# Kernel optimization log

Hardware: AMD Instinct MI355X
Metric: run time of the kernel (lower is better)

## Reference

```python
import jax, jax.numpy as jnp
import numpy as np

N_NODES = 20000
NUM_STEPS = 6
SIGNS = (1.0, -1.0, 1.0, -1.0, 1.0, -1.0)  # TF_POS, TF_NEG, PPI_POS, PPI_NEG, UNDIR, MIRNA_NEG


def setup_inputs() -> dict:
    key = jax.random.key(0)
    ks = jax.random.split(key, 12)
    B, N, E, H, C = 64, N_NODES, 400000, 64, 32
    return {
        "ctl_base": jax.random.normal(ks[0], (B, N), jnp.float32),
        "u_raw": jax.random.normal(ks[1], (B, N), jnp.float32),
        "cell_idx": jax.random.randint(ks[2], (B,), 0, C, jnp.int32),
        "edge_src": jax.random.randint(ks[3], (6, E), 0, N, jnp.int32),
        "edge_dst": jax.random.randint(ks[4], (6, E), 0, N, jnp.int32),
        "edge_val": jax.random.uniform(ks[5], (6, E), jnp.float32),
        "g_logits": jnp.zeros((6,), jnp.float32),
        "alpha_logits": jnp.zeros((NUM_STEPS,), jnp.float32),
        "cell_emb": jax.random.normal(ks[6], (C, H), jnp.float32),
        "W1": jax.random.normal(ks[7], (3, H), jnp.float32) * 0.1,
        "b1": jnp.zeros((H,), jnp.float32),
        "W2": jax.random.normal(ks[8], (H, 1), jnp.float32) * 0.1,
        "b2": jnp.zeros((1,), jnp.float32),
    }


def _spmm_right(h, src, dst, val):
    # out[b, j] = sum_{e: dst[e]==j} h[b, src[e]] * val[e]   (== h @ A)
    gathered = h.T[src] * val[:, None]  # [E, B]
    return jax.ops.segment_sum(gathered, dst, num_segments=N_NODES).T  # [B, N]


def reference(ctl_base, u_raw, g_logits, alpha_logits, cell_emb,
              W1, b1, W2, b2, edge_val, edge_src, edge_dst, cell_idx):
    g = jax.nn.softplus(g_logits)          # [6] relation gates
    alphas = jax.nn.sigmoid(alpha_logits)  # [num_steps]
    h0 = u_raw
    h = u_raw
    for k in range(NUM_STEPS):
        msg = jnp.zeros_like(h)
        for r in range(6):
            msg = msg + SIGNS[r] * g[r] * _spmm_right(h, edge_src[r], edge_dst[r], edge_val[r])
        a = alphas[k]
        h = a * h0 + (1.0 - a) * msg
    # decode: stack [ctl, u_raw, hK] -> [B, N, 3]
    x = jnp.stack([ctl_base, u_raw, h], axis=-1)
    hd = jax.nn.relu(jnp.einsum('bnf,fh->bnh', x, W1) + b1)  # [B, N, H]
    hd = hd + cell_emb[cell_idx][:, None, :]
    y = (jnp.einsum('bnh,ho->bno', hd, W2) + b2)[..., 0]  # [B, N]
    return y
```

## Files before the change

kernel.cpp:

```cpp
#include <hip/hip_runtime.h>

#define N_NODES 20000
#define HID 64
#define NSTEPS 6
#define NSLICE 8
#define SLICE_SZ (N_NODES / NSLICE)
#define SUBB 64
#define NBLK (NSLICE * SUBB)
#define TBLK ((N_NODES + 63) / 64)
#define NB1 512
#define CBLK ((N_NODES + 255) / 256)
#define MAGIC 13422

typedef _Float16 h8_t __attribute__((ext_vector_type(8)));
typedef unsigned u4_t __attribute__((ext_vector_type(4)));

union U16H { unsigned short u; _Float16 h; };
union U4H8 { uint4 u; _Float16 h[8]; };

__device__ __forceinline__ _Float16 us_as_h(unsigned short s) { U16H u; u.u = s; return u.h; }
__device__ __forceinline__ unsigned short h_as_us(_Float16 h) { U16H u; u.h = h; return u.u; }

__device__ __forceinline__ int slice_of(int d) {
    return (int)(((unsigned)d * (unsigned)MAGIC) >> 25);
}
__device__ __forceinline__ float softplusf_(float x) {
    return (x > 0.f) ? (x + log1pf(expf(-x))) : log1pf(expf(x));
}
__device__ __forceinline__ float sigmoidf_(float x) {
    return 1.f / (1.f + expf(-x));
}

__global__ __launch_bounds__(256) void count8_kernel(const int* __restrict__ edst,
                                                     int* __restrict__ gcnt, int TE,
                                                     u4_t* __restrict__ egq, long long egq_n) {
    u4_t z = {0u, 0u, 0u, 0u};
    for (long long i = (long long)blockIdx.x * 256 + threadIdx.x; i < egq_n;
         i += (long long)NB1 * 256)
        __builtin_nontemporal_store(z, egq + i);

    __shared__ int lh[8];
    int bk = blockIdx.x;
    int lane = threadIdx.x & 63;
    if (threadIdx.x < 8) lh[threadIdx.x] = 0;
    __syncthreads();
    int chunk = ((TE + NB1 - 1) / NB1 + 255) & ~255;
    int lo = bk * chunk;
    int hi = min(lo + chunk, TE);
    int my = 0;
    for (int ii = 0; ii < chunk; ii += 256) {
        int i = lo + ii + (int)threadIdx.x;
        bool act = i < hi;
        int s = -1;
        if (act) s = slice_of(__builtin_nontemporal_load(edst + i));
#pragma unroll
        for (int q = 0; q < 8; ++q) {
            unsigned long long b = __ballot(s == q);
            if (lane == q) my += (int)__popcll(b);
        }
    }
    if (lane < 8) atomicAdd(&lh[lane], my);
    __syncthreads();
    if (threadIdx.x < 8) gcnt[bk * 8 + threadIdx.x] = lh[threadIdx.x];
}

__global__ __launch_bounds__(256) void scan8_kernel(const int* __restrict__ gcnt,
                                                    int* __restrict__ blkoff,
                                                    int* __restrict__ bbase,
                                                    const float* __restrict__ g_logits,
                                                    const float* __restrict__ alpha_logits,
                                                    const int* __restrict__ cell_idx,
                                                    const float* __restrict__ cell_emb,
                                                    const float* __restrict__ W2,
                                                    const float* __restrict__ b2,
                                                    float* __restrict__ gsign,
                                                    float* __restrict__ alph,
                                                    float* __restrict__ cell_dot) {
    __shared__ int psum[8][33];
    int tid = threadIdx.x;
    int s = tid >> 5, g = tid & 31;
    const int per = NB1 / 32;
    int sum = 0;
    for (int b = g * per; b < (g + 1) * per; ++b) sum += gcnt[b * 8 + s];
    psum[s][g] = sum;
    __syncthreads();
    if (tid < 8) {
        int run = 0;
        for (int i = 0; i < 32; ++i) { int v = psum[tid][i]; psum[tid][i] = run; run += v; }
        psum[tid][32] = run;
    }
    __syncthreads();
    int run = psum[s][g];
    for (int b = g * per; b < (g + 1) * per; ++b) {
        blkoff[b * 8 + s] = run;
        run += gcnt[b * 8 + s];
    }
    if (tid == 0) {
        int acc = 0;
        bbase[0] = 0;
        for (int q = 0; q < 8; ++q) { acc += psum[q][32]; bbase[q + 1] = acc; }
    }
    if (tid < 64) {
        if (tid < 6) gsign[tid] = ((tid & 1) ? -1.f : 1.f) * softplusf_(g_logits[tid]);
        if (tid < NSTEPS) alph[tid] = sigmoidf_(alpha_logits[tid]);
        int ci = cell_idx[tid];
        float acc = b2[0];
        for (int hh = 0; hh < HID; ++hh) acc = fmaf(cell_emb[ci * HID + hh], W2[hh], acc);
        cell_dot[tid] = acc;
    }
}

__global__ __launch_bounds__(256) void bucket_kernel(const int* __restrict__ esrc,
                                                     const int* __restrict__ edst,
                                                     const float* __restrict__ eval,
                                                     const float* __restrict__ gsign,
                                                     const int* __restrict__ blkoff,
                                                     const int* __restrict__ bbase,
                                                     int2* __restrict__ bucket,
                                                     int E, int TE) {
    __shared__ int lcur[8];
    int bk = blockIdx.x;
    int lane = threadIdx.x & 63;
    if (threadIdx.x < 8) lcur[threadIdx.x] = bbase[threadIdx.x] + blkoff[bk * 8 + threadIdx.x];
    __syncthreads();
    int chunk = ((TE + NB1 - 1) / NB1 + 255) & ~255;
    int lo = bk * chunk;
    int hi = min(lo + chunk, TE);
    for (int ii = 0; ii < chunk; ii += 256) {
        int i = lo + ii + (int)threadIdx.x;
        bool act = i < hi;
        int s = -1, meta = 0, cb = 0;
        if (act) {
            int d  = __builtin_nontemporal_load(edst + i);
            int sv = __builtin_nontemporal_load(esrc + i);
            float ev = __builtin_nontemporal_load(eval + i);
            s = slice_of(d);
            int dl = d - s * SLICE_SZ;
            meta = sv | (dl << 16);
            int r = (i >= E) + (i >= 2 * E) + (i >= 3 * E) + (i >= 4 * E) + (i >= 5 * E);
            cb = __float_as_int(gsign[r] * ev);
        }
        int pos = 0;
#pragma unroll
        for (int q = 0; q < 8; ++q) {
            unsigned long long b = __ballot(s == q);
            if (b) {
                int leader = (int)__ffsll(b) - 1;
                int base = 0;
                if (lane == leader) base = atomicAdd(&lcur[q], (int)__popcll(b));
                base = __shfl(base, leader);
                if (s == q) pos = base + (int)__popcll(b & ((1ull << lane) - 1ull));
            }
        }
        if (act) bucket[pos] = make_int2(meta, cb);
    }
}

__global__ __launch_bounds__(256) void hist2db_kernel(const int2* __restrict__ bucket,
                                                      const int* __restrict__ bbase,
                                                      int* __restrict__ blkcnt) {
    __shared__ int lh[SLICE_SZ];
    int bk = blockIdx.x;
    int slice = bk & (NSLICE - 1);
    int sub = bk >> 3;
    for (int b = threadIdx.x; b < SLICE_SZ; b += 256) lh[b] = 0;
    __syncthreads();
    int lo = bbase[slice];
    int total = bbase[slice + 1] - lo;
    int chunk = ((total + SUBB - 1) / SUBB + 255) & ~255;
    int beg = lo + sub * chunk;
    int end = min(beg + chunk, lo + total);
    const int* mp = (const int*)bucket;
    for (int i = beg + (int)threadIdx.x; i < end; i += 256) {
        int meta = __builtin_nontemporal_load(mp + 2 * (size_t)i);
        atomicAdd(&lh[((unsigned)meta) >> 16], 1);
    }
    __syncthreads();
    int* out = blkcnt + (size_t)(slice * SUBB + sub) * SLICE_SZ;
    for (int b = threadIdx.x; b < SLICE_SZ; b += 256) out[b] = lh[b];
}

__global__ __launch_bounds__(256) void colscan_kernel(int* __restrict__ blkcnt,
                                                      int* __restrict__ counts,
                                                      int* __restrict__ blksum) {
    int n = blockIdx.x * 256 + threadIdx.x;
    int run = 0;
    if (n < N_NODES) {
        int slice = n / SLICE_SZ, bin = n % SLICE_SZ;
        size_t base = (size_t)slice * SUBB * SLICE_SZ + bin;
#pragma unroll 8
        for (int s = 0; s < SUBB; ++s) {
            size_t idx = base + (size_t)s * SLICE_SZ;
            int t = blkcnt[idx];
            blkcnt[idx] = run;
            run += t;
        }
        counts[n] = run;
    }
    int g = (n < N_NODES) ? ((run + 7) >> 3) : 0;
#pragma unroll
    for (int st = 1; st < 64; st <<= 1) g += __shfl_xor(g, st, 64);
    __shared__ int wsum[4];
    if ((threadIdx.x & 63) == 0) wsum[threadIdx.x >> 6] = g;
    __syncthreads();
    if (threadIdx.x == 0) blksum[blockIdx.x] = wsum[0] + wsum[1] + wsum[2] + wsum[3];
}

__global__ __launch_bounds__(256) void scan2_kernel(const int* __restrict__ counts,
                                                    const int* __restrict__ blksum,
                                                    int* __restrict__ grp_ptr, int n) {
    int b = blockIdx.x;
    int tid = threadIdx.x, lane = tid & 63, wid = tid >> 6;
    int i = b * 256 + tid;
    int v = (i < n) ? ((counts[i] + 7) >> 3) : 0;
    int x = v;
#pragma unroll
    for (int st = 1; st < 64; st <<= 1) {
        int t = __shfl_up(x, st, 64);
        if (lane >= st) x += t;
    }
    __shared__ int wsum[4];
    if (lane == 63) wsum[wid] = x;
    int s = ((lane < b) ? blksum[lane] : 0) +
            ((lane + 64 < b) ? blksum[lane + 64] : 0);
#pragma unroll
    for (int st = 1; st < 64; st <<= 1) s += __shfl_xor(s, st, 64);
    __syncthreads();
    int woff = s;
    if (wid > 0) woff += wsum[0];
    if (wid > 1) woff += wsum[1];
    if (wid > 2) woff += wsum[2];
    int off = woff + x - v;
    if (i < n) grp_ptr[i] = off;
    if (i == n - 1) grp_ptr[n] = off + v;
}

__global__ __launch_bounds__(256) void scatter2b_kernel(const int2* __restrict__ bucket,
                                                        const int* __restrict__ bbase,
                                                        const int* __restrict__ grp_ptr,
                                                        const int* __restrict__ blkcnt,
                                                        unsigned* __restrict__ eg,
                                                        const float* __restrict__ u_raw,
                                                        float* __restrict__ u_t,
                                                        _Float16* __restrict__ uh) {
    __shared__ float smem[64 * 65];
    int bk = blockIdx.x;
    if (bk >= NBLK) {
        float(*tile)[65] = (float(*)[65])smem;
        int c0 = (bk - NBLK) * 64;
        int tx = threadIdx.x & 63, ty = threadIdx.x >> 6;
#pragma unroll
        for (int i = 0; i < 16; ++i) {
            int c = c0 + tx;
            tile[ty + i * 4][tx] = (c < N_NODES) ? u_raw[(size_t)(ty + i * 4) * N_NODES + c] : 0.f;
        }
        __syncthreads();
#pragma unroll
        for (int i = 0; i < 16; ++i) {
            int c = c0 + ty + i * 4;
            if (c < N_NODES) {
                float v = tile[tx][ty + i * 4];
                u_t[(size_t)c * 64 + tx] = v;
                uh[(size_t)c * 64 + tx] = (_Float16)v;
            }
        }
        return;
    }
    int* lbase = (int*)smem;
    int slice = bk & (NSLICE - 1);
    int sub = bk >> 3;
    int lo_n = slice * SLICE_SZ;
    const int* boff = blkcnt + (size_t)(slice * SUBB + sub) * SLICE_SZ;
    for (int b = threadIdx.x; b < SLICE_SZ; b += 256)
        lbase[b] = grp_ptr[lo_n + b] * 8 + boff[b];
    __syncthreads();
    int lo = bbase[slice];
    int total = bbase[slice + 1] - lo;
    int chunk = ((total + SUBB - 1) / SUBB + 255) & ~255;
    int beg = lo + sub * chunk;
    int end = min(beg + chunk, lo + total);
    for (int i = beg + (int)threadIdx.x; i < end; i += 256) {
        long long rec = __builtin_nontemporal_load((const long long*)bucket + i);
        int meta = (int)rec;
        float cf = __int_as_float((int)(rec >> 32));
        int pos = atomicAdd(&lbase[((unsigned)meta) >> 16], 1);
        eg[pos] = (unsigned)(meta & 0xFFFF) | ((unsigned)h_as_us((_Float16)cf) << 16);
    }
}

__global__ __launch_bounds__(256) void step_kernel(const _Float16* __restrict__ h_in,
                                                   const float* __restrict__ h0,
                                                   _Float16* __restrict__ h_out,
                                                   float* __restrict__ hF,
                                                   const int* __restrict__ grp_ptr,
                                                   const unsigned* __restrict__ eg,
                                                   const float* __restrict__ alph,
                                                   int k, int last) {
    int lane = threadIdx.x & 63;
    int node = blockIdx.x * 4 + (threadIdx.x >> 6);
    if (node >= N_NODES) return;
    int gb = __builtin_amdgcn_readfirstlane(grp_ptr[node]);
    int ge = __builtin_amdgcn_readfirstlane(grp_ptr[node + 1]);
    int sub8 = lane >> 3;
    const _Float16* hbase = h_in + (lane & 7) * 8;
    const unsigned* ep = eg + sub8;
    float acc[8] = {0.f, 0.f, 0.f, 0.f, 0.f, 0.f, 0.f, 0.f};
    int g = gb;
    unsigned e0, e1, e2, e3;
    if (g + 4 <= ge) {
        e0 = ep[(size_t)g * 8];
        e1 = ep[(size_t)g * 8 + 8];
        e2 = ep[(size_t)g * 8 + 16];
        e3 = ep[(size_t)g * 8 + 24];
    }
    for (; g + 8 <= ge; g += 4) {
        h8_t v0 = *(const h8_t*)(hbase + (e0 & 0xFFFFu) * 64);
        h8_t v1 = *(const h8_t*)(hbase + (e1 & 0xFFFFu) * 64);
        h8_t v2 = *(const h8_t*)(hbase + (e2 & 0xFFFFu) * 64);
        h8_t v3 = *(const h8_t*)(hbase + (e3 & 0xFFFFu) * 64);
        unsigned f0 = ep[(size_t)(g + 4) * 8];
        unsigned f1 = ep[(size_t)(g + 4) * 8 + 8];
        unsigned f2 = ep[(size_t)(g + 4) * 8 + 16];
        unsigned f3 = ep[(size_t)(g + 4) * 8 + 24];
        float c0 = (float)us_as_h((unsigned short)(e0 >> 16));
        float c1 = (float)us_as_h((unsigned short)(e1 >> 16));
        float c2 = (float)us_as_h((unsigned short)(e2 >> 16));
        float c3 = (float)us_as_h((unsigned short)(e3 >> 16));
#pragma unroll
        for (int j = 0; j < 8; ++j) acc[j] = fmaf((float)v0[j], c0, acc[j]);
#pragma unroll
        for (int j = 0; j < 8; ++j) acc[j] = fmaf((float)v1[j], c1, acc[j]);
#pragma unroll
        for (int j = 0; j < 8; ++j) acc[j] = fmaf((float)v2[j], c2, acc[j]);
#pragma unroll
        for (int j = 0; j < 8; ++j) acc[j] = fmaf((float)v3[j], c3, acc[j]);
        e0 = f0; e1 = f1; e2 = f2; e3 = f3;
    }
    if (g + 4 <= ge) {
        h8_t v0 = *(const h8_t*)(hbase + (e0 & 0xFFFFu) * 64);
        h8_t v1 = *(const h8_t*)(hbase + (e1 & 0xFFFFu) * 64);
        h8_t v2 = *(const h8_t*)(hbase + (e2 & 0xFFFFu) * 64);
        h8_t v3 = *(const h8_t*)(hbase + (e3 & 0xFFFFu) * 64);
        float c0 = (float)us_as_h((unsigned short)(e0 >> 16));
        float c1 = (float)us_as_h((unsigned short)(e1 >> 16));
        float c2 = (float)us_as_h((unsigned short)(e2 >> 16));
        float c3 = (float)us_as_h((unsigned short)(e3 >> 16));
#pragma unroll
        for (int j = 0; j < 8; ++j) acc[j] = fmaf((float)v0[j], c0, acc[j]);
#pragma unroll
        for (int j = 0; j < 8; ++j) acc[j] = fmaf((float)v1[j], c1, acc[j]);
#pragma unroll
        for (int j = 0; j < 8; ++j) acc[j] = fmaf((float)v2[j], c2, acc[j]);
#pragma unroll
        for (int j = 0; j < 8; ++j) acc[j] = fmaf((float)v3[j], c3, acc[j]);
        g += 4;
    }
    for (; g < ge; ++g) {
        unsigned e = ep[(size_t)g * 8];
        h8_t v = *(const h8_t*)(hbase + (e & 0xFFFFu) * 64);
        float c = (float)us_as_h((unsigned short)(e >> 16));
#pragma unroll
        for (int j = 0; j < 8; ++j) acc[j] = fmaf((float)v[j], c, acc[j]);
    }
#pragma unroll
    for (int st = 8; st < 64; st <<= 1) {
#pragma unroll
        for (int j = 0; j < 8; ++j) acc[j] += __shfl_xor(acc[j], st, 64);
    }
    if (lane < 8) {
        float a = alph[k];
        int base = node * 64 + lane * 8;
        float4 h0a = *(const float4*)(h0 + base);
        float4 h0b = *(const float4*)(h0 + base + 4);
        float om = 1.f - a;
        float r0 = fmaf(a, h0a.x, om * acc[0]);
        float r1 = fmaf(a, h0a.y, om * acc[1]);
        float r2 = fmaf(a, h0a.z, om * acc[2]);
        float r3 = fmaf(a, h0a.w, om * acc[3]);
        float r4 = fmaf(a, h0b.x, om * acc[4]);
        float r5 = fmaf(a, h0b.y, om * acc[5]);
        float r6 = fmaf(a, h0b.z, om * acc[6]);
        float r7 = fmaf(a, h0b.w, om * acc[7]);
        if (last) {
            *(float4*)(hF + base)     = make_float4(r0, r1, r2, r3);
            *(float4*)(hF + base + 4) = make_float4(r4, r5, r6, r7);
        } else {
            U4H8 o;
            o.h[0] = (_Float16)r0; o.h[1] = (_Float16)r1;
            o.h[2] = (_Float16)r2; o.h[3] = (_Float16)r3;
            o.h[4] = (_Float16)r4; o.h[5] = (_Float16)r5;
            o.h[6] = (_Float16)r6; o.h[7] = (_Float16)r7;
            *(uint4*)(h_out + base) = o.u;
        }
    }
}

__global__ __launch_bounds__(256) void decode_kernel(float* __restrict__ y,
                                                     const float* __restrict__ ctl,
                                                     const float* __restrict__ u,
                                                     const float* __restrict__ hF,
                                                     const float* __restrict__ W1,
                                                     const float* __restrict__ b1,
                                                     const float* __restrict__ W2,
                                                     const float* __restrict__ cell_dot) {
    __shared__ float tile[64][65];
    __shared__ float4 pack[HID];
    __shared__ float w2s[HID];
    __shared__ float cds[64];
    if (threadIdx.x < HID) {
        int hh = threadIdx.x;
        pack[hh] = make_float4(W1[0 * HID + hh], W1[1 * HID + hh], W1[2 * HID + hh], b1[hh]);
        w2s[hh] = W2[hh];
        cds[hh] = cell_dot[hh];
    }
    int n0 = blockIdx.x * 64;
    int tx = threadIdx.x & 63, ty = threadIdx.x >> 6;
#pragma unroll
    for (int i = 0; i < 16; ++i) {
        int n = n0 + ty + i * 4;
        tile[ty + i * 4][tx] = (n < N_NODES) ? hF[(size_t)n * 64 + tx] : 0.f;
    }
    __syncthreads();
#pragma unroll
    for (int i = 0; i < 16; ++i) {
        int b = ty + i * 4;
        int n = n0 + tx;
        if (n < N_NODES) {
            size_t idx = (size_t)b * N_NODES + n;
            float xc = ctl[idx], xu = u[idx], xh = tile[tx][b];
            float acc = 0.f;
#pragma unroll 8
            for (int hh = 0; hh < HID; ++hh) {
                float4 p = pack[hh];
                float t = fmaf(xc, p.x, fmaf(xu, p.y, fmaf(xh, p.z, p.w)));
                t = fmaxf(t, 0.f);
                acc = fmaf(t, w2s[hh], acc);
            }
            y[idx] = acc + cds[b];
        }
    }
}

extern "C" void kernel_launch(void* const* d_in, const int* in_sizes, int n_in,
                              void* d_out, int out_size, void* d_ws, size_t ws_size,
                              hipStream_t stream) {
    const float* ctl          = (const float*)d_in[0];
    const float* u_raw        = (const float*)d_in[1];
    const int*   cell_idx     = (const int*)d_in[2];
    const int*   edge_src     = (const int*)d_in[3];
    const int*   edge_dst     = (const int*)d_in[4];
    const float* edge_val     = (const float*)d_in[5];
    const float* g_logits     = (const float*)d_in[6];
    const float* alpha_logits = (const float*)d_in[7];
    const float* cell_emb     = (const float*)d_in[8];
    const float* W1           = (const float*)d_in[9];
    const float* b1           = (const float*)d_in[10];
    const float* W2           = (const float*)d_in[11];
    const float* b2           = (const float*)d_in[12];
    float* y = (float*)d_out;

    const int TE = in_sizes[3];
    const int E  = TE / 6;
    const int NB = N_NODES * 64;

    char* ws = (char*)d_ws;
    size_t off = 0;
    auto alloc = [&](size_t bytes) -> char* {
        char* p = ws + off;
        off += (bytes + 255) & ~(size_t)255;
        return p;
    };
    int* grp_ptr = (int*)alloc((N_NODES + 1) * sizeof(int));
    int* counts  = (int*)alloc(N_NODES * sizeof(int));
    int* blksum  = (int*)alloc(CBLK * sizeof(int));
    int* blkcnt  = (int*)alloc((size_t)NSLICE * SUBB * SLICE_SZ * sizeof(int));
    int* gcnt    = (int*)alloc((size_t)NB1 * 8 * sizeof(int));
    int* blkoff  = (int*)alloc((size_t)NB1 * 8 * sizeof(int));
    int* bbase   = (int*)alloc(16 * sizeof(int));
    const size_t MAXG = (size_t)TE / 8 + N_NODES + 8;
    unsigned* eg = (unsigned*)alloc(MAXG * 8 * sizeof(unsigned));
    int2* bucket    = (int2*)alloc((size_t)TE * sizeof(int2));
    _Float16* uh    = (_Float16*)alloc((size_t)NB * 2);
    _Float16* hA    = (_Float16*)alloc((size_t)NB * 2);
    _Float16* hB    = (_Float16*)alloc((size_t)NB * 2);
    float* hF       = (float*)alloc((size_t)NB * 4);
    float* u_t      = (float*)alloc((size_t)NB * sizeof(float));
    float* gsign    = (float*)alloc(8 * sizeof(float));
    float* alph     = (float*)alloc(8 * sizeof(float));
    float* cell_dot = (float*)alloc(64 * sizeof(float));

    count8_kernel<<<NB1, 256, 0, stream>>>(edge_dst, gcnt, TE,
                                           (u4_t*)eg, (long long)(MAXG * 2));
    scan8_kernel<<<1, 256, 0, stream>>>(gcnt, blkoff, bbase, g_logits, alpha_logits,
                                        cell_idx, cell_emb, W2, b2,
                                        gsign, alph, cell_dot);
    bucket_kernel<<<NB1, 256, 0, stream>>>(edge_src, edge_dst, edge_val, gsign,
                                           blkoff, bbase, bucket, E, TE);
    hist2db_kernel<<<NBLK, 256, 0, stream>>>(bucket, bbase, blkcnt);
    colscan_kernel<<<CBLK, 256, 0, stream>>>(blkcnt, counts, blksum);
    scan2_kernel<<<CBLK, 256, 0, stream>>>(counts, blksum, grp_ptr, N_NODES);
    scatter2b_kernel<<<NBLK + TBLK, 256, 0, stream>>>(bucket, bbase, grp_ptr, blkcnt,
                                                      eg, u_raw, u_t, uh);

    const _Float16* hin = uh;
    for (int k = 0; k < NSTEPS; ++k) {
        _Float16* hout = (k & 1) ? hB : hA;
        step_kernel<<<(N_NODES + 3) / 4, 256, 0, stream>>>(hin, u_t, hout, hF, grp_ptr,
                                                           eg, alph, k, k == NSTEPS - 1);
        hin = hout;
    }

    decode_kernel<<<TBLK, 256, 0, stream>>>(y, ctl, u_raw, hF, W1, b1, W2, cell_dot);
}
```

Before: 341.3 us.

## Interleave edge groups into 32-edge quads for uint4 edge loads and deeper gather pipelining

Edge lists per node are padded to multiples of 32 and written in an interleaved order so each 8-lane subgroup can fetch four consecutive edges with one 128-bit load. The step kernel is rewritten into a two-stage software pipeline that keeps two sets of four gathered h rows in flight while the edge loads for the next stages are prefetched. This aims to cut the number of edge-load instructions and hide gather latency. The cost is more padding (up to 31 extra zero edges per node), which adds wasted gathers, a larger edge buffer, and higher register use.

Measured after the change: 352.7 us. 1.03x slower.

```diff
diff --git a/kernel.cpp b/kernel.cpp
--- a/kernel.cpp
+++ b/kernel.cpp
@@ -197,7 +197,7 @@
         }
         counts[n] = run;
     }
-    int g = (n < N_NODES) ? ((run + 7) >> 3) : 0;
+    int g = (n < N_NODES) ? (((run + 31) >> 5) << 2) : 0;
 #pragma unroll
     for (int st = 1; st < 64; st <<= 1) g += __shfl_xor(g, st, 64);
     __shared__ int wsum[4];
@@ -212,7 +212,7 @@
     int b = blockIdx.x;
     int tid = threadIdx.x, lane = tid & 63, wid = tid >> 6;
     int i = b * 256 + tid;
-    int v = (i < n) ? ((counts[i] + 7) >> 3) : 0;
+    int v = (i < n) ? (((counts[i] + 31) >> 5) << 2) : 0;
     int x = v;
 #pragma unroll
     for (int st = 1; st < 64; st <<= 1) {
@@ -267,12 +267,16 @@
         return;
     }
     int* lbase = (int*)smem;
+    int* sbase = (int*)smem + SLICE_SZ;
     int slice = bk & (NSLICE - 1);
     int sub = bk >> 3;
     int lo_n = slice * SLICE_SZ;
     const int* boff = blkcnt + (size_t)(slice * SUBB + sub) * SLICE_SZ;
-    for (int b = threadIdx.x; b < SLICE_SZ; b += 256)
-        lbase[b] = grp_ptr[lo_n + b] * 8 + boff[b];
+    for (int b = threadIdx.x; b < SLICE_SZ; b += 256) {
+        int gp = grp_ptr[lo_n + b] * 8;
+        sbase[b] = gp;
+        lbase[b] = gp + boff[b];
+    }
     __syncthreads();
     int lo = bbase[slice];
     int total = bbase[slice + 1] - lo;
@@ -283,8 +287,12 @@
         long long rec = __builtin_nontemporal_load((const long long*)bucket + i);
         int meta = (int)rec;
         float cf = __int_as_float((int)(rec >> 32));
-        int pos = atomicAdd(&lbase[((unsigned)meta) >> 16], 1);
-        eg[pos] = (unsigned)(meta & 0xFFFF) | ((unsigned)h_as_us((_Float16)cf) << 16);
+        int bin = ((unsigned)meta) >> 16;
+        int pos = atomicAdd(&lbase[bin], 1);
+        int sb = sbase[bin];
+        int j = pos - sb;
+        int npos = sb + (j & ~31) + ((j & 7) << 2) + ((j >> 3) & 3);
+        eg[npos] = (unsigned)(meta & 0xFFFF) | ((unsigned)h_as_us((_Float16)cf) << 16);
     }
 }
 
@@ -301,67 +309,62 @@
     if (node >= N_NODES) return;
     int gb = __builtin_amdgcn_readfirstlane(grp_ptr[node]);
     int ge = __builtin_amdgcn_readfirstlane(grp_ptr[node + 1]);
+    int NQ = (ge - gb) >> 2;
     int sub8 = lane >> 3;
     const _Float16* hbase = h_in + (lane & 7) * 8;
-    const unsigned* ep = eg + sub8;
+    const unsigned* egq = eg + (size_t)gb * 8 + sub8 * 4;
     float acc[8] = {0.f, 0.f, 0.f, 0.f, 0.f, 0.f, 0.f, 0.f};
-    int g = gb;
-    unsigned e0, e1, e2, e3;
-    if (g + 4 <= ge) {
-        e0 = ep[(size_t)g * 8];
-        e1 = ep[(size_t)g * 8 + 8];
-        e2 = ep[(size_t)g * 8 + 16];
-        e3 = ep[(size_t)g * 8 + 24];
-    }
-    for (; g + 8 <= ge; g += 4) {
-        h8_t v0 = *(const h8_t*)(hbase + (e0 & 0xFFFFu) * 64);
-        h8_t v1 = *(const h8_t*)(hbase + (e1 & 0xFFFFu) * 64);
-        h8_t v2 = *(const h8_t*)(hbase + (e2 & 0xFFFFu) * 64);
-        h8_t v3 = *(const h8_t*)(hbase + (e3 & 0xFFFFu) * 64);
-        unsigned f0 = ep[(size_t)(g + 4) * 8];
-        unsigned f1 = ep[(size_t)(g + 4) * 8 + 8];
-        unsigned f2 = ep[(size_t)(g + 4) * 8 + 16];
-        unsigned f3 = ep[(size_t)(g + 4) * 8 + 24];
-        float c0 = (float)us_as_h((unsigned short)(e0 >> 16));
-        float c1 = (float)us_as_h((unsigned short)(e1 >> 16));
-        float c2 = (float)us_as_h((unsigned short)(e2 >> 16));
-        float c3 = (float)us_as_h((unsigned short)(e3 >> 16));
-#pragma unroll
-        for (int j = 0; j < 8; ++j) acc[j] = fmaf((float)v0[j], c0, acc[j]);
-#pragma unroll
-        for (int j = 0; j < 8; ++j) acc[j] = fmaf((float)v1[j], c1, acc[j]);
-#pragma unroll
-        for (int j = 0; j < 8; ++j) acc[j] = fmaf((float)v2[j], c2, acc[j]);
-#pragma unroll
-        for (int j = 0; j < 8; ++j) acc[j] = fmaf((float)v3[j], c3, acc[j]);
-        e0 = f0; e1 = f1; e2 = f2; e3 = f3;
-    }
-    if (g + 4 <= ge) {
-        h8_t v0 = *(const h8_t*)(hbase + (e0 & 0xFFFFu) * 64);
-        h8_t v1 = *(const h8_t*)(hbase + (e1 & 0xFFFFu) * 64);
-        h8_t v2 = *(const h8_t*)(hbase + (e2 & 0xFFFFu) * 64);
-        h8_t v3 = *(const h8_t*)(hbase + (e3 & 0xFFFFu) * 64);
-        float c0 = (float)us_as_h((unsigned short)(e0 >> 16));
-        float c1 = (float)us_as_h((unsigned short)(e1 >> 16));
-        float c2 = (float)us_as_h((unsigned short)(e2 >> 16));
-        float c3 = (float)us_as_h((unsigned short)(e3 >> 16));
-#pragma unroll
-        for (int j = 0; j < 8; ++j) acc[j] = fmaf((float)v0[j], c0, acc[j]);
-#pragma unroll
-        for (int j = 0; j < 8; ++j) acc[j] = fmaf((float)v1[j], c1, acc[j]);
-#pragma unroll
-        for (int j = 0; j < 8; ++j) acc[j] = fmaf((float)v2[j], c2, acc[j]);
-#pragma unroll
-        for (int j = 0; j < 8; ++j) acc[j] = fmaf((float)v3[j], c3, acc[j]);
-        g += 4;
-    }
-    for (; g < ge; ++g) {
-        unsigned e = ep[(size_t)g * 8];
-        h8_t v = *(const h8_t*)(hbase + (e & 0xFFFFu) * 64);
-        float c = (float)us_as_h((unsigned short)(e >> 16));
-#pragma unroll
-        for (int j = 0; j < 8; ++j) acc[j] = fmaf((float)v[j], c, acc[j]);
-    }
+
+#define LDE(Q) (*(const uint4*)(egq + (size_t)(Q) * 32))
+#define GATH(e) (*(const h8_t*)(hbase + ((e) & 0xFFFFu) * 64))
+#define FMA4(V0, V1, V2, V3, EE)                                              \
+    do {                                                                      \
+        float c0 = (float)us_as_h((unsigned short)((EE).x >> 16));            \
+        float c1 = (float)us_as_h((unsigned short)((EE).y >> 16));            \
+        float c2 = (float)us_as_h((unsigned short)((EE).z >> 16));            \
+        float c3 = (float)us_as_h((unsigned short)((EE).w >> 16));            \
+        _Pragma("unroll") for (int j = 0; j < 8; ++j)                         \
+            acc[j] = fmaf((float)(V0)[j], c0, acc[j]);                        \
+        _Pragma("unroll") for (int j = 0; j < 8; ++j)                         \
+            acc[j] = fmaf((float)(V1)[j], c1, acc[j]);                        \
+        _Pragma("unroll") for (int j = 0; j < 8; ++j)                         \
+            acc[j] = fmaf((float)(V2)[j], c2, acc[j]);                        \
+        _Pragma("unroll") for (int j = 0; j < 8; ++j)                         \
+            acc[j] = fmaf((float)(V3)[j], c3, acc[j]);                        \
+    } while (0)
+
+    uint4 e0, e1, e2;
+    h8_t A0, A1, A2, A3, B0, B1, B2, B3;
+    if (NQ > 0) {
+        e0 = LDE(0);
+        e1 = LDE(1);
+        e2 = LDE(2);
+        A0 = GATH(e0.x); A1 = GATH(e0.y); A2 = GATH(e0.z); A3 = GATH(e0.w);
+    }
+    int q = 0;
+    for (; q + 2 < NQ; q += 2) {
+        B0 = GATH(e1.x); B1 = GATH(e1.y); B2 = GATH(e1.z); B3 = GATH(e1.w);
+        uint4 e3 = LDE(q + 3);
+        FMA4(A0, A1, A2, A3, e0);
+        A0 = GATH(e2.x); A1 = GATH(e2.y); A2 = GATH(e2.z); A3 = GATH(e2.w);
+        uint4 e4 = LDE(q + 4);
+        FMA4(B0, B1, B2, B3, e1);
+        e0 = e2; e1 = e3; e2 = e4;
+    }
+    int r = NQ - q;
+    if (r > 0) {
+        if (r > 1) {
+            B0 = GATH(e1.x); B1 = GATH(e1.y); B2 = GATH(e1.z); B3 = GATH(e1.w);
+            FMA4(A0, A1, A2, A3, e0);
+            FMA4(B0, B1, B2, B3, e1);
+        } else {
+            FMA4(A0, A1, A2, A3, e0);
+        }
+    }
+#undef LDE
+#undef GATH
+#undef FMA4
+
 #pragma unroll
     for (int st = 8; st < 64; st <<= 1) {
 #pragma unroll
@@ -477,7 +480,7 @@
     int* gcnt    = (int*)alloc((size_t)NB1 * 8 * sizeof(int));
     int* blkoff  = (int*)alloc((size_t)NB1 * 8 * sizeof(int));
     int* bbase   = (int*)alloc(16 * sizeof(int));
-    const size_t MAXG = (size_t)TE / 8 + N_NODES + 8;
+    const size_t MAXG = (size_t)TE / 8 + 4 * (size_t)N_NODES + 64;
     unsigned* eg = (unsigned*)alloc(MAXG * 8 * sizeof(unsigned));
     int2* bucket    = (int2*)alloc((size_t)TE * sizeof(int2));
     _Float16* uh    = (_Float16*)alloc((size_t)NB * 2);
```
